# Performance work log

Measured on AMD Instinct MI355X. Metric: run time of the kernel, lower is better.

Reference implementation:

```python
import jax, jax.numpy as jnp
import numpy as np

K = 20  # neighbors, from init kwarg k

def _knn_idx(x, k):
    # x: [B, C, N]; returns indices of k nearest neighbors [B, N, k]
    xx = jnp.sum(x * x, axis=1)                      # [B, N]
    inner = jnp.einsum('bcn,bcm->bnm', x, x)         # [B, N, N]
    neg_dist = 2.0 * inner - xx[:, :, None] - xx[:, None, :]
    return jax.lax.top_k(neg_dist, k)[1]


def _graph_feature(x, k):
    # x: [B, C, N] -> [B, N, k, 2C] = concat(neighbor - center, center)
    idx = _knn_idx(jax.lax.stop_gradient(x), k)
    xt = jnp.swapaxes(x, 1, 2)                       # [B, N, C]
    nb = jax.vmap(lambda pts, i: pts[i])(xt, idx)    # [B, N, k, C]
    ctr = jnp.broadcast_to(xt[:, :, None, :], nb.shape)
    return jnp.concatenate([nb - ctr, ctr], axis=-1)


def _edge_conv(x, layers, k):
    # x: [B, C, N]; layers: list of (w [Co,Ci], scale [Co], bias [Co])
    g = _graph_feature(x, k)                         # [B, N, k, 2C]
    for w, s, b in layers:
        g = jax.nn.leaky_relu(jnp.einsum('bnkc,oc->bnko', g, w) * s + b, 0.2)
    return jnp.swapaxes(jnp.max(g, axis=2), 1, 2)    # [B, Co, N]


def setup_inputs() -> dict:
    key = jax.random.key(0)
    ks = jax.random.split(key, 20)
    B, N = 2, 8192
    emb = 1024
    def w(k_, shape):
        fan_in = shape[1]
        return jax.random.normal(k_, shape, jnp.float32) * (1.0 / np.sqrt(fan_in))
    def sc(k_, c):
        return jax.random.uniform(k_, (c,), jnp.float32, 0.5, 1.5)
    def bi(k_, c):
        return jax.random.normal(k_, (c,), jnp.float32) * 0.1
    inp = {
        'points': jax.random.normal(ks[0], (B, N, 3), jnp.float32),
        'w1a': w(ks[1], (64, 12)),  's1a': sc(ks[2], 64),  'b1a': bi(ks[3], 64),
        'w1b': w(ks[4], (64, 64)),  's1b': sc(ks[5], 64),  'b1b': bi(ks[6], 64),
        'w2a': w(ks[7], (64, 128)), 's2a': sc(ks[8], 64),  'b2a': bi(ks[9], 64),
        'w2b': w(ks[10], (64, 64)), 's2b': sc(ks[11], 64), 'b2b': bi(ks[12], 64),
        'w3a': w(ks[13], (64, 128)),'s3a': sc(ks[14], 64), 'b3a': bi(ks[15], 64),
        'wg':  w(ks[16], (emb, 192)),'sg': sc(ks[17], emb),'bg': bi(ks[18], emb),
    }
    return inp


def reference(points, w1a, s1a, b1a, w1b, s1b, b1b,
              w2a, s2a, b2a, w2b, s2b, b2b,
              w3a, s3a, b3a, wg, sg, bg):
    B, N, _ = points.shape
    xyz = jnp.swapaxes(points, 1, 2)                 # [B, 3, N]
    x = jnp.concatenate([xyz, xyz], axis=1)          # [B, 6, N] (features == xyz when C==3)
    x1 = _edge_conv(x,  [(w1a, s1a, b1a), (w1b, s1b, b1b)], K)
    x2 = _edge_conv(x1, [(w2a, s2a, b2a), (w2b, s2b, b2b)], K)
    x3 = _edge_conv(x2, [(w3a, s3a, b3a)], K)
    cat = jnp.concatenate([x1, x2, x3], axis=1)      # [B, 192, N]
    h = jax.nn.leaky_relu(
        jnp.einsum('bcn,oc->bon', cat, wg) * sg[None, :, None] + bg[None, :, None], 0.2)
    g = jnp.max(h, axis=-1, keepdims=True)           # [B, emb, 1]
    x_max = jnp.broadcast_to(g, (B, h.shape[1], N))  # [B, emb, N]
    return x_max
```

## Files before the change

kernel.cpp:

```cpp
#include <hip/hip_runtime.h>
#include <hip/hip_bf16.h>

#define NPTS 8192
#define KNN  20
#define KC   4

__device__ __forceinline__ unsigned fkey(float f) {
  unsigned u = __float_as_uint(f);
  return (u & 0x80000000u) ? ~u : (u | 0x80000000u);
}
__device__ __forceinline__ float funkey(unsigned k) {
  return (k & 0x80000000u) ? __uint_as_float(k & 0x7fffffffu) : __uint_as_float(~k);
}
__device__ __forceinline__ float lrelu(float x) { return x >= 0.f ? x : 0.2f * x; }

__global__ __launch_bounds__(256) void prep_kernel(
    const float* __restrict__ w1a, const float* __restrict__ w1b,
    const float* __restrict__ w2a, const float* __restrict__ w2b,
    const float* __restrict__ w3a, const float* __restrict__ wg,
    float* __restrict__ wp1A, float* __restrict__ wp1B,
    float* __restrict__ wp2A, float* __restrict__ wp2B,
    float* __restrict__ wp3A, float* __restrict__ wgT)
{
  const int t0 = blockIdx.x * blockDim.x + threadIdx.x;
  const int NT = gridDim.x * blockDim.x;
  for (int f = t0; f < 512; f += NT) {
    int i = f & 3, o = (f >> 2) & 63, c4 = f >> 8, c = c4 * 4 + i;
    float v = 0.f;
    if (c < 3)      v = w1a[o*12 + c]     + w1a[o*12 + c + 3];
    else if (c < 6) v = w1a[o*12 + c + 3] + w1a[o*12 + c + 6];
    wp1A[f] = v;
  }
  for (int f = t0; f < 4096; f += NT) {
    int i = f & 3, o = (f >> 2) & 63, c4 = f >> 8, c = c4 * 4 + i;
    wp1B[f] = w1b[o*64 + c];
    wp2B[f] = w2b[o*64 + c];
  }
  for (int f = t0; f < 8192; f += NT) {
    int i = f & 3, o = (f >> 2) & 63, c4 = f >> 8, c = c4 * 4 + i;
    wp2A[f] = w2a[o*128 + c];
    wp3A[f] = w3a[o*128 + c];
  }
  for (int f = t0; f < 192 * 1024; f += NT) {
    int c = f >> 10, o = f & 1023;
    wgT[f] = wg[o*192 + c];
  }
}

__global__ __launch_bounds__(256) void xx_points(const float* __restrict__ pts,
                                                 float* __restrict__ xx)
{
  int t = blockIdx.x * 256 + threadIdx.x;
  if (t < 2 * NPTS) {
    const float* p = pts + (size_t)t * 3;
    xx[t] = p[0]*p[0] + p[1]*p[1] + p[2]*p[2];
  }
}

__device__ __forceinline__ void bitonic64_desc_f(float& v, int lane) {
  #pragma unroll
  for (int k = 2; k <= 64; k <<= 1) {
    #pragma unroll
    for (int j = k >> 1; j >= 1; j >>= 1) {
      float o = __shfl_xor(v, j);
      bool take_max = (((lane & k) == 0) == ((lane & j) == 0));
      v = take_max ? fmaxf(v, o) : fminf(v, o);
    }
  }
}

__device__ __forceinline__ void bitonic64_desc_u64(unsigned long long& v, int lane) {
  #pragma unroll
  for (int k = 2; k <= 64; k <<= 1) {
    #pragma unroll
    for (int j = k >> 1; j >= 1; j >>= 1) {
      unsigned long long o = __shfl_xor(v, j);
      bool take_max = (((lane & k) == 0) == ((lane & j) == 0));
      unsigned long long hi = v > o ? v : o;
      unsigned long long lo = v > o ? o : v;
      v = take_max ? hi : lo;
    }
  }
}

__device__ void select20_fast(float* __restrict__ sdrow, int lane,
                              int* __restrict__ orow,
                              float* __restrict__ cv, int* __restrict__ cj)
{
  float m = -INFINITY;
  const float4* rp = (const float4*)(sdrow + lane * 128);
  #pragma unroll
  for (int t = 0; t < 32; ++t) {
    float4 x = rp[(t + lane) & 31];
    m = fmaxf(m, fmaxf(fmaxf(x.x, x.y), fmaxf(x.z, x.w)));
  }
  bitonic64_desc_f(m, lane);
  float That = __shfl(m, 19);

  int base = 0;
  for (int i = 0; i < 128; ++i) {
    float v = sdrow[i * 64 + lane];
    bool p = (v >= That);
    unsigned long long mk = __ballot(p);
    if (p) {
      int pos = base + (int)__popcll(mk & ((1ull << lane) - 1ull));
      if (pos < 64) { cv[pos] = v; cj[pos] = i * 64 + lane; }
    }
    base += (int)__popcll(mk);
  }

  if (base <= 64) {
    unsigned long long key = 0ull;
    if (lane < base)
      key = (((unsigned long long)fkey(cv[lane])) << 32) | (unsigned)(~cj[lane]);
    bitonic64_desc_u64(key, lane);
    if (lane < KNN) orow[lane] = (int)((~(unsigned)key) & (NPTS - 1));
  } else {
    for (int kk = 0; kk < KNN; ++kk) {
      float bv = -INFINITY; int bj = NPTS;
      for (int i = 0; i < 128; ++i) {
        float v = sdrow[i * 64 + lane];
        if (v > bv) { bv = v; bj = i * 64 + lane; }
      }
      #pragma unroll
      for (int mm = 32; mm >= 1; mm >>= 1) {
        float ov = __shfl_xor(bv, mm); int oj = __shfl_xor(bj, mm);
        if (ov > bv || (ov == bv && oj < bj)) { bv = ov; bj = oj; }
      }
      if (lane == 0) orow[kk] = bj;
      sdrow[bj] = -INFINITY;
    }
  }
}

__global__ __launch_bounds__(512, 2) void knn3_kernel(
    const float* __restrict__ pts, const float* __restrict__ xx,
    int* __restrict__ idxout)
{
  __shared__ __align__(16) float sd[4][NPTS];
  __shared__ float s_ctr[4][4];
  __shared__ float s_cv[4][64];
  __shared__ int   s_cj[4][64];
  const int tid = threadIdx.x;
  const int b   = blockIdx.x / (NPTS / 4);
  const int r0  = (blockIdx.x % (NPTS / 4)) * 4;
  const size_t rowbase = (size_t)b * NPTS;

  for (int i = tid; i < 12; i += 512)
    s_ctr[i / 3][i % 3] = pts[(rowbase + r0 + i / 3) * 3 + i % 3];
  __syncthreads();

  const float xr0 = xx[rowbase + r0 + 0], xr1 = xx[rowbase + r0 + 1];
  const float xr2 = xx[rowbase + r0 + 2], xr3 = xx[rowbase + r0 + 3];
  const float c00 = s_ctr[0][0], c01 = s_ctr[0][1], c02 = s_ctr[0][2];
  const float c10 = s_ctr[1][0], c11 = s_ctr[1][1], c12 = s_ctr[1][2];
  const float c20 = s_ctr[2][0], c21 = s_ctr[2][1], c22 = s_ctr[2][2];
  const float c30 = s_ctr[3][0], c31 = s_ctr[3][1], c32 = s_ctr[3][2];

  for (int j = tid; j < NPTS; j += 512) {
    const float* fj = pts + (rowbase + j) * 3;
    const float f0 = fj[0], f1 = fj[1], f2 = fj[2];
    const float xj = xx[rowbase + j];
    sd[0][j] = 2.f*(f0*c00 + f1*c01 + f2*c02) - xr0 - xj;
    sd[1][j] = 2.f*(f0*c10 + f1*c11 + f2*c12) - xr1 - xj;
    sd[2][j] = 2.f*(f0*c20 + f1*c21 + f2*c22) - xr2 - xj;
    sd[3][j] = 2.f*(f0*c30 + f1*c31 + f2*c32) - xr3 - xj;
  }
  __syncthreads();

  const int wid = tid >> 6, lane = tid & 63;
  if (wid < 4)
    select20_fast(sd[wid], lane, idxout + (rowbase + r0 + wid) * KNN,
                  s_cv[wid], s_cj[wid]);
}

#define ACC4(A, C) \
  A.x += v0.x*C.x + v1.x*C.y + v2.x*C.z + v3.x*C.w; \
  A.y += v0.y*C.x + v1.y*C.y + v2.y*C.z + v3.y*C.w; \
  A.z += v0.z*C.x + v1.z*C.y + v2.z*C.z + v3.z*C.w; \
  A.w += v0.w*C.x + v1.w*C.y + v2.w*C.z + v3.w*C.w;

__global__ __launch_bounds__(512, 2) void knn64_kernel(
    const float* __restrict__ featT, const float* __restrict__ xx,
    int* __restrict__ idxout)
{
  __shared__ __align__(16) float sd[4][NPTS];
  __shared__ __align__(16) float s_ctr[4][64];
  __shared__ float s_cv[4][64];
  __shared__ int   s_cj[4][64];
  const int tid = threadIdx.x;
  const int bid = blockIdx.x;
  const int b   = (bid & 7) >> 2;
  const int r0  = (((bid >> 3) << 2) + (bid & 3)) * 4;
  const size_t tb = (size_t)b * 64 * NPTS;
  const size_t rowbase = (size_t)b * NPTS;

  if (tid < 256)
    s_ctr[tid >> 6][tid & 63] = featT[tb + (size_t)(tid & 63) * NPTS + r0 + (tid >> 6)];
  __syncthreads();

  const int wid = tid >> 6, lane = tid & 63;
  const float xr0 = xx[rowbase + r0 + 0], xr1 = xx[rowbase + r0 + 1];
  const float xr2 = xx[rowbase + r0 + 2], xr3 = xx[rowbase + r0 + 3];
  const float4* ct0 = (const float4*)s_ctr[0];
  const float4* ct1 = (const float4*)s_ctr[1];
  const float4* ct2 = (const float4*)s_ctr[2];
  const float4* ct3 = (const float4*)s_ctr[3];

  #pragma unroll 1
  for (int ch = 0; ch < 4; ++ch) {
    const int jb = (wid << 10) + (ch << 8) + (lane << 2);
    float4 a0 = {0.f,0.f,0.f,0.f}, a1 = a0, a2 = a0, a3 = a0;
    const float* fp0 = featT + tb + jb;
    #pragma unroll 4
    for (int c4 = 0; c4 < 16; ++c4) {
      const float* fp = fp0 + (size_t)(c4 * 4) * NPTS;
      float4 v0 = *(const float4*)(fp);
      float4 v1 = *(const float4*)(fp + NPTS);
      float4 v2 = *(const float4*)(fp + 2 * NPTS);
      float4 v3 = *(const float4*)(fp + 3 * NPTS);
      float4 c0 = ct0[c4], c1 = ct1[c4], c2 = ct2[c4], c3 = ct3[c4];
      ACC4(a0, c0); ACC4(a1, c1); ACC4(a2, c2); ACC4(a3, c3);
    }
    const float4 xv = *(const float4*)(xx + rowbase + jb);
    float4 s0, s1, s2, s3;
    s0.x = 2.f*a0.x - xr0 - xv.x; s0.y = 2.f*a0.y - xr0 - xv.y;
    s0.z = 2.f*a0.z - xr0 - xv.z; s0.w = 2.f*a0.w - xr0 - xv.w;
    s1.x = 2.f*a1.x - xr1 - xv.x; s1.y = 2.f*a1.y - xr1 - xv.y;
    s1.z = 2.f*a1.z - xr1 - xv.z; s1.w = 2.f*a1.w - xr1 - xv.w;
    s2.x = 2.f*a2.x - xr2 - xv.x; s2.y = 2.f*a2.y - xr2 - xv.y;
    s2.z = 2.f*a2.z - xr2 - xv.z; s2.w = 2.f*a2.w - xr2 - xv.w;
    s3.x = 2.f*a3.x - xr3 - xv.x; s3.y = 2.f*a3.y - xr3 - xv.y;
    s3.z = 2.f*a3.z - xr3 - xv.z; s3.w = 2.f*a3.w - xr3 - xv.w;
    *(float4*)&sd[0][jb] = s0;
    *(float4*)&sd[1][jb] = s1;
    *(float4*)&sd[2][jb] = s2;
    *(float4*)&sd[3][jb] = s3;
  }
  __syncthreads();

  if (wid < 4)
    select20_fast(sd[wid], lane, idxout + (rowbase + r0 + wid) * KNN,
                  s_cv[wid], s_cj[wid]);
}

template<int D, bool HASB, bool WAUX>
__global__ __launch_bounds__(256) void fused_conv(
    const float* __restrict__ feat, int fstride, int foff,
    const int* __restrict__ idx,
    const float4* __restrict__ wAp, const float* __restrict__ sa, const float* __restrict__ ba,
    const float4* __restrict__ wBp, const float* __restrict__ sb, const float* __restrict__ bb,
    float* __restrict__ outbuf, int ooff, float* __restrict__ xxout,
    float* __restrict__ featT)
{
  constexpr int CHA  = (D == 64) ? 32 : 2;
  constexpr int CHA4 = CHA * 4;
  __shared__ float4 s_wA[CHA * 64];
  __shared__ float4 s_wB[HASB ? 16 * 64 : 1];
  __shared__ __align__(16) float4 s_g[4 * KC * CHA];
  __shared__ __align__(16) float  s_h1[HASB ? 4 * KC * 64 : 4];
  __shared__ float s_ctr[4][(D > 4) ? D : 4];
  __shared__ float s_sa[64], s_ba[64], s_sb[64], s_bb[64];

  const int tid = threadIdx.x;
  const int p = tid >> 6, o = tid & 63;
  const int b  = blockIdx.x / (NPTS / 4);
  const int p0 = (blockIdx.x % (NPTS / 4)) * 4;
  const size_t rowbase = (size_t)b * NPTS;

  for (int i = tid; i < CHA * 64; i += 256) s_wA[i] = wAp[i];
  if (HASB) for (int i = tid; i < 16 * 64; i += 256) s_wB[i] = wBp[i];
  if (tid < 64) {
    s_sa[tid] = sa[tid]; s_ba[tid] = ba[tid];
    if (HASB) { s_sb[tid] = sb[tid]; s_bb[tid] = bb[tid]; }
  }
  for (int i = tid; i < 4 * D; i += 256)
    s_ctr[i / D][i % D] = feat[(rowbase + p0 + (i / D)) * fstride + foff + (i % D)];
  __syncthreads();

  float* s_gf = (float*)s_g;
  float hmax = -INFINITY;
  for (int kc = 0; kc < KNN / KC; ++kc) {
    for (int s = tid; s < 4 * KC * CHA4; s += 256) {
      int pp = s / (KC * CHA4);
      int rr = s - pp * (KC * CHA4);
      int kk = rr / CHA4;
      int c  = rr - kk * CHA4;
      int nb = idx[(rowbase + p0 + pp) * KNN + kc * KC + kk];
      float v;
      if (D == 64) {
        v = (c < 64) ? (feat[(rowbase + nb) * fstride + foff + c] - s_ctr[pp][c])
                     : s_ctr[pp][c - 64];
      } else {
        if (c < 3)      v = feat[(rowbase + nb) * 3 + c] - s_ctr[pp][c];
        else if (c < 6) v = s_ctr[pp][c - 3];
        else            v = 0.f;
      }
      s_gf[s] = v;
    }
    __syncthreads();

    float acc[KC];
    #pragma unroll
    for (int kk = 0; kk < KC; ++kk) acc[kk] = 0.f;
    for (int c4 = 0; c4 < CHA; ++c4) {
      float4 w = s_wA[c4 * 64 + o];
      #pragma unroll
      for (int kk = 0; kk < KC; ++kk) {
        float4 g = s_g[(p * KC + kk) * CHA + c4];
        acc[kk] += w.x*g.x + w.y*g.y + w.z*g.z + w.w*g.w;
      }
    }
    if (HASB) {
      #pragma unroll
      for (int kk = 0; kk < KC; ++kk)
        s_h1[(p * KC + kk) * 64 + o] = lrelu(acc[kk] * s_sa[o] + s_ba[o]);
      __syncthreads();
      float acc2[KC];
      #pragma unroll
      for (int kk = 0; kk < KC; ++kk) acc2[kk] = 0.f;
      const float4* s_h14 = (const float4*)s_h1;
      for (int c4 = 0; c4 < 16; ++c4) {
        float4 w = s_wB[c4 * 64 + o];
        #pragma unroll
        for (int kk = 0; kk < KC; ++kk) {
          float4 h = s_h14[(p * KC + kk) * 16 + c4];
          acc2[kk] += w.x*h.x + w.y*h.y + w.z*h.z + w.w*h.w;
        }
      }
      #pragma unroll
      for (int kk = 0; kk < KC; ++kk)
        hmax = fmaxf(hmax, lrelu(acc2[kk] * s_sb[o] + s_bb[o]));
      __syncthreads();
    } else {
      #pragma unroll
      for (int kk = 0; kk < KC; ++kk)
        hmax = fmaxf(hmax, lrelu(acc[kk] * s_sa[o] + s_ba[o]));
      __syncthreads();
    }
  }
  outbuf[(rowbase + p0 + p) * 192 + ooff + o] = hmax;
  if (WAUX) {
    featT[(size_t)b * 64 * NPTS + (size_t)o * NPTS + (p0 + p)] = hmax;
    float ss = hmax * hmax;
    #pragma unroll
    for (int m = 1; m < 64; m <<= 1) ss += __shfl_xor(ss, m);
    if (o == 0) xxout[rowbase + p0 + p] = ss;
  }
}

__global__ __launch_bounds__(256) void init_gmax(unsigned* __restrict__ g)
{
  int t = blockIdx.x * 256 + threadIdx.x;
  if (t < 2048) g[t] = fkey(-1e30f);
}

__global__ __launch_bounds__(256) void final_kernel(
    const float* __restrict__ cat, const float* __restrict__ wgT,
    const float* __restrict__ sg, const float* __restrict__ bg,
    unsigned* __restrict__ gmax)
{
  const int tid = threadIdx.x;
  const int chunk = blockIdx.x & 15;
  const int grp   = blockIdx.x >> 4;
  const int pt = grp * 256 + tid;
  const int b  = pt >> 13;
  const float4* crow = (const float4*)(cat + (size_t)pt * 192);
  float acc[64];
  #pragma unroll
  for (int o = 0; o < 64; ++o) acc[o] = 0.f;
  for (int c4 = 0; c4 < 48; ++c4) {
    float4 cv = crow[c4];
    const float* w0 = wgT + (size_t)(c4 * 4) * 1024 + chunk * 64;
    const float* w1 = w0 + 1024;
    const float* w2 = w1 + 1024;
    const float* w3 = w2 + 1024;
    #pragma unroll
    for (int o = 0; o < 64; ++o)
      acc[o] += cv.x*w0[o] + cv.y*w1[o] + cv.z*w2[o] + cv.w*w3[o];
  }
  const int lane = tid & 63;
  #pragma unroll
  for (int o = 0; o < 64; ++o) {
    int ch = chunk * 64 + o;
    float h = lrelu(acc[o] * sg[ch] + bg[ch]);
    #pragma unroll
    for (int m = 1; m < 64; m <<= 1) h = fmaxf(h, __shfl_xor(h, m));
    if (lane == 0) atomicMax(&gmax[b * 1024 + ch], fkey(h));
  }
}

__global__ __launch_bounds__(256) void bcast_kernel(const unsigned* __restrict__ gmax,
                                                    float* __restrict__ out)
{
  int t = blockIdx.x * 256 + threadIdx.x;
  int bo = t >> 11;
  float v = funkey(gmax[bo]);
  float4 w; w.x = v; w.y = v; w.z = v; w.w = v;
  ((float4*)out)[t] = w;
}

extern "C" void kernel_launch(void* const* d_in, const int* in_sizes, int n_in,
                              void* d_out, int out_size, void* d_ws, size_t ws_size,
                              hipStream_t stream)
{
  const float* points = (const float*)d_in[0];
  const float* w1a = (const float*)d_in[1];  const float* s1a = (const float*)d_in[2];  const float* b1a = (const float*)d_in[3];
  const float* w1b = (const float*)d_in[4];  const float* s1b = (const float*)d_in[5];  const float* b1b = (const float*)d_in[6];
  const float* w2a = (const float*)d_in[7];  const float* s2a = (const float*)d_in[8];  const float* b2a = (const float*)d_in[9];
  const float* w2b = (const float*)d_in[10]; const float* s2b = (const float*)d_in[11]; const float* b2b = (const float*)d_in[12];
  const float* w3a = (const float*)d_in[13]; const float* s3a = (const float*)d_in[14]; const float* b3a = (const float*)d_in[15];
  const float* wg  = (const float*)d_in[16]; const float* sg  = (const float*)d_in[17]; const float* bg  = (const float*)d_in[18];

  char* ws = (char*)d_ws;
  float*    cat   = (float*)(ws);
  float*    xxbuf = (float*)(ws + 12582912);
  int*      idxb  = (int*)  (ws + 12648448);
  float*    wp1A  = (float*)(ws + 13959168);
  float*    wp1B  = (float*)(ws + 13961216);
  float*    wp2A  = (float*)(ws + 13977600);
  float*    wp2B  = (float*)(ws + 14010368);
  float*    wp3A  = (float*)(ws + 14026752);
  float*    wgT   = (float*)(ws + 14059520);
  unsigned* gmax  = (unsigned*)(ws + 14845952);
  const size_t WS_NEED = 14854144;
  if (ws_size < WS_NEED || n_in != 19) return;

  float* featT = (float*)d_out;

  prep_kernel<<<256, 256, 0, stream>>>(w1a, w1b, w2a, w2b, w3a, wg,
                                       wp1A, wp1B, wp2A, wp2B, wp3A, wgT);
  xx_points<<<64, 256, 0, stream>>>(points, xxbuf);
  knn3_kernel<<<4096, 512, 0, stream>>>(points, xxbuf, idxb);
  fused_conv<3, true, true><<<4096, 256, 0, stream>>>(
      points, 3, 0, idxb, (const float4*)wp1A, s1a, b1a,
      (const float4*)wp1B, s1b, b1b, cat, 0, xxbuf, featT);
  knn64_kernel<<<4096, 512, 0, stream>>>(featT, xxbuf, idxb);
  fused_conv<64, true, true><<<4096, 256, 0, stream>>>(
      cat, 192, 0, idxb, (const float4*)wp2A, s2a, b2a,
      (const float4*)wp2B, s2b, b2b, cat, 64, xxbuf, featT);
  knn64_kernel<<<4096, 512, 0, stream>>>(featT, xxbuf, idxb);
  fused_conv<64, false, false><<<4096, 256, 0, stream>>>(
      cat, 192, 64, idxb, (const float4*)wp3A, s3a, b3a,
      nullptr, nullptr, nullptr, cat, 128, nullptr, nullptr);
  init_gmax<<<8, 256, 0, stream>>>(gmax);
  final_kernel<<<1024, 256, 0, stream>>>(cat, wgT, sg, bg, gmax);
  bcast_kernel<<<16384, 256, 0, stream>>>(gmax, (float*)d_out);
}
```

Before: 2.046 ms.

## Split kNN distance rows into halves to halve LDS and raise occupancy

The kNN kernels now compute distances for 4096 columns at a time into a half-size shared buffer. Each half gets its own top-20 selection, and the two candidate lists are merged with a bitonic sort, which cuts LDS per block from 128KB to about 64KB. The launch bound rises from 2 to 4 blocks per CU so more warps can overlap memory and selection work. In exchange it adds an extra selection pass, more barriers, and a merge step, while the 4 of 8 waves left idle during selection stay idle.

```diff
diff --git a/kernel.cpp b/kernel.cpp
--- a/kernel.cpp
+++ b/kernel.cpp
@@ -83,23 +83,23 @@
   }
 }
 
-__device__ void select20_fast(float* __restrict__ sdrow, int lane,
-                              int* __restrict__ orow,
-                              float* __restrict__ cv, int* __restrict__ cj)
+__device__ void sel20_half(float* __restrict__ sdh, int half, int lane,
+                           float* __restrict__ hv, int* __restrict__ hj,
+                           float* __restrict__ cv, int* __restrict__ cj)
 {
   float m = -INFINITY;
-  const float4* rp = (const float4*)(sdrow + lane * 128);
+  const float4* rp = (const float4*)(sdh + lane * 64);
   #pragma unroll
-  for (int t = 0; t < 32; ++t) {
-    float4 x = rp[(t + lane) & 31];
+  for (int t = 0; t < 16; ++t) {
+    float4 x = rp[(t + lane) & 15];
     m = fmaxf(m, fmaxf(fmaxf(x.x, x.y), fmaxf(x.z, x.w)));
   }
   bitonic64_desc_f(m, lane);
   float That = __shfl(m, 19);
 
   int base = 0;
-  for (int i = 0; i < 128; ++i) {
-    float v = sdrow[i * 64 + lane];
+  for (int i = 0; i < 64; ++i) {
+    float v = sdh[i * 64 + lane];
     bool p = (v >= That);
     unsigned long long mk = __ballot(p);
     if (p) {
@@ -114,12 +114,15 @@
     if (lane < base)
       key = (((unsigned long long)fkey(cv[lane])) << 32) | (unsigned)(~cj[lane]);
     bitonic64_desc_u64(key, lane);
-    if (lane < KNN) orow[lane] = (int)((~(unsigned)key) & (NPTS - 1));
+    if (lane < KNN) {
+      hv[lane] = funkey((unsigned)(key >> 32));
+      hj[lane] = (half << 12) + (int)((~(unsigned)key) & 4095u);
+    }
   } else {
     for (int kk = 0; kk < KNN; ++kk) {
-      float bv = -INFINITY; int bj = NPTS;
-      for (int i = 0; i < 128; ++i) {
-        float v = sdrow[i * 64 + lane];
+      float bv = -INFINITY; int bj = 4096;
+      for (int i = 0; i < 64; ++i) {
+        float v = sdh[i * 64 + lane];
         if (v > bv) { bv = v; bj = i * 64 + lane; }
       }
       #pragma unroll
@@ -127,18 +130,31 @@
         float ov = __shfl_xor(bv, mm); int oj = __shfl_xor(bj, mm);
         if (ov > bv || (ov == bv && oj < bj)) { bv = ov; bj = oj; }
       }
-      if (lane == 0) orow[kk] = bj;
-      sdrow[bj] = -INFINITY;
-    }
-  }
-}
-
-__global__ __launch_bounds__(512, 2) void knn3_kernel(
+      if (lane == 0) { hv[kk] = bv; hj[kk] = (half << 12) + bj; }
+      sdh[bj] = -INFINITY;
+    }
+  }
+}
+
+__device__ __forceinline__ void merge_halves(const float* __restrict__ hv,
+                                             const int* __restrict__ hj,
+                                             int lane, int* __restrict__ orow)
+{
+  unsigned long long key = 0ull;
+  if (lane < 2 * KNN)
+    key = (((unsigned long long)fkey(hv[lane])) << 32) | (unsigned)(~hj[lane]);
+  bitonic64_desc_u64(key, lane);
+  if (lane < KNN) orow[lane] = (int)((~(unsigned)key) & (NPTS - 1));
+}
+
+__global__ __launch_bounds__(512, 4) void knn3_kernel(
     const float* __restrict__ pts, const float* __restrict__ xx,
     int* __restrict__ idxout)
 {
-  __shared__ __align__(16) float sd[4][NPTS];
+  __shared__ __align__(16) float sd[4][4096];
   __shared__ float s_ctr[4][4];
+  __shared__ float s_hv[4][2 * KNN];
+  __shared__ int   s_hj[4][2 * KNN];
   __shared__ float s_cv[4][64];
   __shared__ int   s_cj[4][64];
   const int tid = threadIdx.x;
@@ -156,22 +172,28 @@
   const float c10 = s_ctr[1][0], c11 = s_ctr[1][1], c12 = s_ctr[1][2];
   const float c20 = s_ctr[2][0], c21 = s_ctr[2][1], c22 = s_ctr[2][2];
   const float c30 = s_ctr[3][0], c31 = s_ctr[3][1], c32 = s_ctr[3][2];
-
-  for (int j = tid; j < NPTS; j += 512) {
-    const float* fj = pts + (rowbase + j) * 3;
-    const float f0 = fj[0], f1 = fj[1], f2 = fj[2];
-    const float xj = xx[rowbase + j];
-    sd[0][j] = 2.f*(f0*c00 + f1*c01 + f2*c02) - xr0 - xj;
-    sd[1][j] = 2.f*(f0*c10 + f1*c11 + f2*c12) - xr1 - xj;
-    sd[2][j] = 2.f*(f0*c20 + f1*c21 + f2*c22) - xr2 - xj;
-    sd[3][j] = 2.f*(f0*c30 + f1*c31 + f2*c32) - xr3 - xj;
-  }
-  __syncthreads();
-
   const int wid = tid >> 6, lane = tid & 63;
+
+  #pragma unroll 1
+  for (int h = 0; h < 2; ++h) {
+    for (int jl = tid; jl < 4096; jl += 512) {
+      const int jg = (h << 12) + jl;
+      const float* fj = pts + (rowbase + jg) * 3;
+      const float f0 = fj[0], f1 = fj[1], f2 = fj[2];
+      const float xj = xx[rowbase + jg];
+      sd[0][jl] = 2.f*(f0*c00 + f1*c01 + f2*c02) - xr0 - xj;
+      sd[1][jl] = 2.f*(f0*c10 + f1*c11 + f2*c12) - xr1 - xj;
+      sd[2][jl] = 2.f*(f0*c20 + f1*c21 + f2*c22) - xr2 - xj;
+      sd[3][jl] = 2.f*(f0*c30 + f1*c31 + f2*c32) - xr3 - xj;
+    }
+    __syncthreads();
+    if (wid < 4)
+      sel20_half(sd[wid], h, lane, &s_hv[wid][h * KNN], &s_hj[wid][h * KNN],
+                 s_cv[wid], s_cj[wid]);
+    __syncthreads();
+  }
   if (wid < 4)
-    select20_fast(sd[wid], lane, idxout + (rowbase + r0 + wid) * KNN,
-                  s_cv[wid], s_cj[wid]);
+    merge_halves(s_hv[wid], s_hj[wid], lane, idxout + (rowbase + r0 + wid) * KNN);
 }
 
 #define ACC4(A, C) \
@@ -180,12 +202,14 @@
   A.z += v0.z*C.x + v1.z*C.y + v2.z*C.z + v3.z*C.w; \
   A.w += v0.w*C.x + v1.w*C.y + v2.w*C.z + v3.w*C.w;
 
-__global__ __launch_bounds__(512, 2) void knn64_kernel(
+__global__ __launch_bounds__(512, 4) void knn64_kernel(
     const float* __restrict__ featT, const float* __restrict__ xx,
     int* __restrict__ idxout)
 {
-  __shared__ __align__(16) float sd[4][NPTS];
+  __shared__ __align__(16) float sd[4][4096];
   __shared__ __align__(16) float s_ctr[4][64];
+  __shared__ float s_hv[4][2 * KNN];
+  __shared__ int   s_hj[4][2 * KNN];
   __shared__ float s_cv[4][64];
   __shared__ int   s_cj[4][64];
   const int tid = threadIdx.x;
@@ -208,40 +232,46 @@
   const float4* ct3 = (const float4*)s_ctr[3];
 
   #pragma unroll 1
-  for (int ch = 0; ch < 4; ++ch) {
-    const int jb = (wid << 10) + (ch << 8) + (lane << 2);
-    float4 a0 = {0.f,0.f,0.f,0.f}, a1 = a0, a2 = a0, a3 = a0;
-    const float* fp0 = featT + tb + jb;
-    #pragma unroll 4
-    for (int c4 = 0; c4 < 16; ++c4) {
-      const float* fp = fp0 + (size_t)(c4 * 4) * NPTS;
-      float4 v0 = *(const float4*)(fp);
-      float4 v1 = *(const float4*)(fp + NPTS);
-      float4 v2 = *(const float4*)(fp + 2 * NPTS);
-      float4 v3 = *(const float4*)(fp + 3 * NPTS);
-      float4 c0 = ct0[c4], c1 = ct1[c4], c2 = ct2[c4], c3 = ct3[c4];
-      ACC4(a0, c0); ACC4(a1, c1); ACC4(a2, c2); ACC4(a3, c3);
-    }
-    const float4 xv = *(const float4*)(xx + rowbase + jb);
-    float4 s0, s1, s2, s3;
-    s0.x = 2.f*a0.x - xr0 - xv.x; s0.y = 2.f*a0.y - xr0 - xv.y;
-    s0.z = 2.f*a0.z - xr0 - xv.z; s0.w = 2.f*a0.w - xr0 - xv.w;
-    s1.x = 2.f*a1.x - xr1 - xv.x; s1.y = 2.f*a1.y - xr1 - xv.y;
-    s1.z = 2.f*a1.z - xr1 - xv.z; s1.w = 2.f*a1.w - xr1 - xv.w;
-    s2.x = 2.f*a2.x - xr2 - xv.x; s2.y = 2.f*a2.y - xr2 - xv.y;
-    s2.z = 2.f*a2.z - xr2 - xv.z; s2.w = 2.f*a2.w - xr2 - xv.w;
-    s3.x = 2.f*a3.x - xr3 - xv.x; s3.y = 2.f*a3.y - xr3 - xv.y;
-    s3.z = 2.f*a3.z - xr3 - xv.z; s3.w = 2.f*a3.w - xr3 - xv.w;
-    *(float4*)&sd[0][jb] = s0;
-    *(float4*)&sd[1][jb] = s1;
-    *(float4*)&sd[2][jb] = s2;
-    *(float4*)&sd[3][jb] = s3;
-  }
-  __syncthreads();
-
+  for (int h = 0; h < 2; ++h) {
+    #pragma unroll 1
+    for (int ch = 0; ch < 2; ++ch) {
+      const int jl = (wid << 9) + (ch << 8) + (lane << 2);
+      const int jg = (h << 12) + jl;
+      float4 a0 = {0.f,0.f,0.f,0.f}, a1 = a0, a2 = a0, a3 = a0;
+      const float* fp0 = featT + tb + jg;
+      #pragma unroll 4
+      for (int c4 = 0; c4 < 16; ++c4) {
+        const float* fp = fp0 + (size_t)(c4 * 4) * NPTS;
+        float4 v0 = *(const float4*)(fp);
+        float4 v1 = *(const float4*)(fp + NPTS);
+        float4 v2 = *(const float4*)(fp + 2 * NPTS);
+        float4 v3 = *(const float4*)(fp + 3 * NPTS);
+        float4 c0 = ct0[c4], c1 = ct1[c4], c2 = ct2[c4], c3 = ct3[c4];
+        ACC4(a0, c0); ACC4(a1, c1); ACC4(a2, c2); ACC4(a3, c3);
+      }
+      const float4 xv = *(const float4*)(xx + rowbase + jg);
+      float4 s0, s1, s2, s3;
+      s0.x = 2.f*a0.x - xr0 - xv.x; s0.y = 2.f*a0.y - xr0 - xv.y;
+      s0.z = 2.f*a0.z - xr0 - xv.z; s0.w = 2.f*a0.w - xr0 - xv.w;
+      s1.x = 2.f*a1.x - xr1 - xv.x; s1.y = 2.f*a1.y - xr1 - xv.y;
+      s1.z = 2.f*a1.z - xr1 - xv.z; s1.w = 2.f*a1.w - xr1 - xv.w;
+      s2.x = 2.f*a2.x - xr2 - xv.x; s2.y = 2.f*a2.y - xr2 - xv.y;
+      s2.z = 2.f*a2.z - xr2 - xv.z; s2.w = 2.f*a2.w - xr2 - xv.w;
+      s3.x = 2.f*a3.x - xr3 - xv.x; s3.y = 2.f*a3.y - xr3 - xv.y;
+      s3.z = 2.f*a3.z - xr3 - xv.z; s3.w = 2.f*a3.w - xr3 - xv.w;
+      *(float4*)&sd[0][jl] = s0;
+      *(float4*)&sd[1][jl] = s1;
+      *(float4*)&sd[2][jl] = s2;
+      *(float4*)&sd[3][jl] = s3;
+    }
+    __syncthreads();
+    if (wid < 4)
+      sel20_half(sd[wid], h, lane, &s_hv[wid][h * KNN], &s_hj[wid][h * KNN],
+                 s_cv[wid], s_cj[wid]);
+    __syncthreads();
+  }
   if (wid < 4)
-    select20_fast(sd[wid], lane, idxout + (rowbase + r0 + wid) * KNN,
-                  s_cv[wid], s_cj[wid]);
+    merge_halves(s_hv[wid], s_hj[wid], lane, idxout + (rowbase + r0 + wid) * KNN);
 }
 
 template<int D, bool HASB, bool WAUX>
```

Measured after the change: 1.845 ms. 1.11x faster.
